# Kernel optimization log

Hardware: AMD Instinct MI355X
Metric: run time of the kernel (lower is better)

## Reference

```python
import jax, jax.numpy as jnp
import numpy as np

IN_FEATURES = 512
OUT_FEATURES = 1024
BATCH = 1024
LAMBD = 0.2
TOL = 1e-4
MAX_ITERS = 100


def setup_inputs() -> dict:
    key = jax.random.key(0)
    kx, kw = jax.random.split(key)
    x = jax.random.normal(kx, (BATCH, IN_FEATURES), dtype=jnp.float32)
    # weight ~ randn(out, in), normalized over dim=0 (per-column) as in torch
    w = jax.random.normal(kw, (OUT_FEATURES, IN_FEATURES), dtype=jnp.float32)
    w = w / jnp.linalg.norm(w, axis=0)
    # M_inv = inverse(A^T A + I)^T with A = weight.T of shape (N, M)
    A = w.T  # (N, M)
    Mmat = A.T @ A + jnp.eye(OUT_FEATURES, dtype=jnp.float32)  # (M, M)
    M_inv = jnp.linalg.inv(Mmat).T
    return {"x": x, "weight": w, "M_inv": M_inv}


def _softshrink(x, lambd):
    return jnp.sign(x) * jnp.maximum(jnp.abs(x) - lambd, 0.0)


def _admm(A_dot_b, M_inv, lambd):
    # Fixed-length scan with per-sample freeze masks, equivalent to the
    # torch loop that removes converged rows from the active batch.
    B, M = A_dot_b.shape
    z = jnp.zeros((B, M), A_dot_b.dtype)
    solved0 = jnp.zeros((B,), dtype=bool)
    # carry: (v, u, v_prev, v_solution, solved)
    def step(carry, _):
        v, u, v_prev, v_sol, solved = carry
        b_eff = A_dot_b + v - u               # (B, M)
        xk = b_eff @ M_inv                    # (B, M)
        v_new = _softshrink(xk + u, lambd)
        u_new = u + xk - v_new
        dx_norm = jnp.linalg.norm(v_new - v_prev, axis=1)
        x_norm = jnp.linalg.norm(v_new, axis=1)
        conv = (dx_norm / x_norm) < TOL       # nan (0/0) compares False, as torch
        newly = conv & (~solved)
        v_sol = jnp.where(newly[:, None], v_new, v_sol)
        solved = solved | newly
        active = ~solved
        # frozen (solved) rows stop updating, mirroring removal from the batch
        v2 = jnp.where(active[:, None], v_new, v)
        u2 = jnp.where(active[:, None], u_new, u)
        return (v2, u2, v2, v_sol, solved), None

    carry0 = (z, z, z, z, solved0)
    (v, u, v_prev, v_sol, solved), _ = jax.lax.scan(step, carry0, None, length=MAX_ITERS)
    # torch returns v_solution (zeros for never-converged samples)
    return v_sol


def reference(x, weight, M_inv):
    input_shape = x.shape
    b = jax.lax.stop_gradient(x.reshape(x.shape[0], -1))  # x.detach().flatten(1)
    A_dot_b = b @ weight.T  # b @ A with A = weight.T -> (B, M)
    encoded = _admm(A_dot_b, M_inv, LAMBD)  # (B, M)
    decoded = encoded @ weight              # (B, N)
    return encoded, decoded.reshape(input_shape)
```

## Files before the change

### kernel.cpp

```cpp
#include <hip/hip_runtime.h>

typedef _Float16 half8 __attribute__((ext_vector_type(8)));
typedef _Float16 half4 __attribute__((ext_vector_type(4)));
typedef float floatx4 __attribute__((ext_vector_type(4)));
typedef float floatx16 __attribute__((ext_vector_type(16)));

static constexpr int BATCH = 1024;
static constexpr int NIN   = 512;
static constexpr int MOUT  = 1024;
static constexpr float LAMBD = 0.2f;
static constexpr float TOLF  = 1e-4f;
static constexpr int MAX_ITERS = 100;
static constexpr int MM = BATCH * MOUT;

__device__ __forceinline__ size_t swz(int idx, int k) {
    return ((((size_t)(idx >> 4) * 32 + (k >> 5)) * 64 +
             ((idx & 15) | (((k >> 3) & 3) << 4))) << 3) + (k & 7);
}

__device__ __forceinline__ size_t swz32(int idx, int k) {
    return ((((size_t)(idx >> 5) * 64 + (k >> 4)) * 64 +
             ((idx & 31) | (((k >> 3) & 1) << 5))) << 3) + (k & 7);
}

__device__ __forceinline__ float shrinkf(float t) {
    float a = fabsf(t) - LAMBD;
    return a > 0.f ? copysignf(a, t) : 0.f;
}

__device__ __forceinline__ void gbar32(int* cnt, int* gen, int seq) {
    __syncthreads();
    if (threadIdx.x == 0) {
        int old = atomicAdd(cnt, 1);
        if (old == seq * 32 - 1) {
            __hip_atomic_store(gen, seq, __ATOMIC_RELAXED,
                               __HIP_MEMORY_SCOPE_AGENT);
        } else {
            while (__hip_atomic_load(gen, __ATOMIC_RELAXED,
                                     __HIP_MEMORY_SCOPE_AGENT) < seq)
                __builtin_amdgcn_s_sleep(1);
        }
    }
    __syncthreads();
    asm volatile("buffer_inv sc0" ::: "memory");
}

__global__ __launch_bounds__(256) void zero_init(float* t, float* enc,
                                                 float* dec, float* ench_f,
                                                 float* encl_f, int* solved) {
    int i = blockIdx.x * 256 + threadIdx.x;
    if (i < MM) { t[i] = 0.f; enc[i] = 0.f; }
    if (i < MM / 2) { dec[i] = 0.f; ench_f[i] = 0.f; encl_f[i] = 0.f; }
    if (i < 4096) solved[i] = 0;
}

__global__ __launch_bounds__(256) void split_minv(const float* __restrict__ Minv,
                                                  _Float16* __restrict__ Th,
                                                  _Float16* __restrict__ Tl) {
    int g = blockIdx.x * 256 + threadIdx.x;
    int n = g & 1023, k0 = (g >> 10) << 3;
    half8 h, l;
    #pragma unroll
    for (int e = 0; e < 8; ++e) {
        float val = Minv[(size_t)(k0 + e) * MOUT + n];
        _Float16 hh = (_Float16)val;
        h[e] = hh;
        l[e] = (_Float16)(val - (float)hh);
    }
    size_t off = swz32(n, k0);
    *(half8*)&Th[off] = h;
    *(half8*)&Tl[off] = l;
}

__global__ __launch_bounds__(256) void split_w(const float* __restrict__ w,
                                               _Float16* __restrict__ wsh,
                                               _Float16* __restrict__ wsl) {
    int g = blockIdx.x * 256 + threadIdx.x;
    int n = g & 511, k0 = (g >> 9) << 3;
    half8 h, l;
    #pragma unroll
    for (int e = 0; e < 8; ++e) {
        float val = w[(size_t)(k0 + e) * NIN + n];
        _Float16 hh = (_Float16)val;
        h[e] = hh;
        l[e] = (_Float16)(val - (float)hh);
    }
    size_t off = swz(n, k0);
    *(half8*)&wsh[off] = h;
    *(half8*)&wsl[off] = l;
}

__global__ __launch_bounds__(256) void gemm_adb(const float* __restrict__ x,
                                                const float* __restrict__ w,
                                                float* __restrict__ adb,
                                                _Float16* __restrict__ bh,
                                                _Float16* __restrict__ bl) {
    __shared__ float As[16][68];
    __shared__ float Bs[16][68];
    const int tid = threadIdx.x;
    const int i0 = (blockIdx.x >> 4) * 64, j0 = (blockIdx.x & 15) * 64;
    const int tx = tid & 15, ty = tid >> 4;
    const int lr = tid >> 2, lk = (tid & 3) << 2;
    float acc[4][4] = {};
    for (int k0 = 0; k0 < NIN; k0 += 16) {
        float4 a4 = *(const float4*)&x[(i0 + lr) * NIN + k0 + lk];
        As[lk + 0][lr] = a4.x; As[lk + 1][lr] = a4.y;
        As[lk + 2][lr] = a4.z; As[lk + 3][lr] = a4.w;
        float4 b4 = *(const float4*)&w[(j0 + lr) * NIN + k0 + lk];
        Bs[lk + 0][lr] = b4.x; Bs[lk + 1][lr] = b4.y;
        Bs[lk + 2][lr] = b4.z; Bs[lk + 3][lr] = b4.w;
        __syncthreads();
        #pragma unroll
        for (int kk = 0; kk < 16; ++kk) {
            float4 a_ = *(const float4*)&As[kk][ty << 2];
            float4 b_ = *(const float4*)&Bs[kk][tx << 2];
            #pragma unroll
            for (int r = 0; r < 4; ++r) {
                float av = r == 0 ? a_.x : r == 1 ? a_.y : r == 2 ? a_.z : a_.w;
                acc[r][0] = fmaf(av, b_.x, acc[r][0]);
                acc[r][1] = fmaf(av, b_.y, acc[r][1]);
                acc[r][2] = fmaf(av, b_.z, acc[r][2]);
                acc[r][3] = fmaf(av, b_.w, acc[r][3]);
            }
        }
        __syncthreads();
    }
    const int k4 = j0 + (tx << 2);
    #pragma unroll
    for (int r = 0; r < 4; ++r) {
        const int row = i0 + (ty << 2) + r;
        *(float4*)&adb[(size_t)row * MOUT + k4] =
            make_float4(acc[r][0], acc[r][1], acc[r][2], acc[r][3]);
        half4 h, l;
        #pragma unroll
        for (int e = 0; e < 4; ++e) {
            _Float16 hh = (_Float16)acc[r][e];
            h[e] = hh;
            l[e] = (_Float16)(acc[r][e] - (float)hh);
        }
        size_t off = swz32(row, k4);
        *(half4*)&bh[off] = h;
        *(half4*)&bl[off] = l;
    }
}

__global__ __launch_bounds__(512, 1)
void admm_loop(const float* __restrict__ adb, float* __restrict__ part,
               _Float16* __restrict__ bh0, _Float16* __restrict__ bl0,
               _Float16* __restrict__ bh1, _Float16* __restrict__ bl1,
               const _Float16* __restrict__ Th, const _Float16* __restrict__ Tl,
               float* __restrict__ enc, _Float16* __restrict__ ench,
               _Float16* __restrict__ encl, int* __restrict__ bar) {
    const int bid = blockIdx.x;
    const int tid = threadIdx.x, lane = tid & 63;
    const int w = tid >> 6;
    const int bt = w >> 1;
    const int kh = w & 1;
    const int mt = bid & 7, nt = bid >> 3;
    const int n0 = nt << 5, m0 = mt << 7;
    const int hn = lane >> 5;
    const int brow = m0 + (bt << 5) + (lane & 31);
    const int btile = (mt << 2) + bt;

    __shared__ _Float16 Bs[128 * 512];
    __shared__ float4 sc4[4][4][64];
    __shared__ unsigned char sfroz[128];

    if (tid < 128) sfroz[tid] = 0;

    #pragma unroll
    for (int q = 0; q < 16; ++q) {
        const int chunk = (w << 4) + q;
        const int kc = chunk >> 1, hl = chunk & 1;
        const _Float16* src = (hl ? Tl : Th) +
            (((size_t)((nt << 6) + kc)) << 9) + ((size_t)lane << 3);
        __builtin_amdgcn_global_load_lds(
            (const __attribute__((address_space(1))) void*)src,
            (__attribute__((address_space(3))) void*)&Bs[(size_t)chunk << 9],
            16, 0, 0);
    }
    __syncthreads();

    int* gcnt = bar + (mt << 5);
    int* ggen = bar + (mt << 5) + 16;

    const int drow_l = (w << 4) + (lane >> 2);
    const int dq = (lane & 3) << 3;
    const float* dbase0 = part + ((((size_t)(m0 + drow_l)) << 6) + (dq << 1));

    float treg[16] = {};
    float adbreg[16];
    #pragma unroll
    for (int r4 = 0; r4 < 4; ++r4) {
        const int nb = n0 + (r4 << 3) + (hn << 2);
        float4 a4 = *(const float4*)&adb[(size_t)brow * MOUT + nb];
        adbreg[(r4 << 2) + 0] = a4.x; adbreg[(r4 << 2) + 1] = a4.y;
        adbreg[(r4 << 2) + 2] = a4.z; adbreg[(r4 << 2) + 3] = a4.w;
    }

    int it = 0;
    for (; it < MAX_ITERS; ++it) {
        const _Float16* rbh = (it & 1) ? bh1 : bh0;
        const _Float16* rbl = (it & 1) ? bl1 : bl0;
        _Float16* wbh = (it & 1) ? bh0 : bh1;
        _Float16* wbl = (it & 1) ? bl0 : bl1;
        const int pw = it & 1;

        float4 dp0, dp1, dp2, dp3;
        if (it) {
            const float* pb = dbase0 + ((size_t)(pw ^ 1) << 16);
            dp0 = *(const float4*)(pb + 0);
            dp1 = *(const float4*)(pb + 4);
            dp2 = *(const float4*)(pb + 8);
            dp3 = *(const float4*)(pb + 12);
        }

        floatx16 accA = {}, accB = {}, accC = {};
        const int kc0 = kh << 5;
        #pragma unroll 4
        for (int kc = kc0; kc < kc0 + 32; ++kc) {
            const size_t boff =
                (((size_t)(btile << 6) + kc) << 9) + ((size_t)lane << 3);
            const half8 bhf = *(const half8*)&rbh[boff];
            const half8 blf = *(const half8*)&rbl[boff];
            const half8 ah = *(const half8*)&Bs[((kc << 1) << 9) + (lane << 3)];
            const half8 al = *(const half8*)&Bs[(((kc << 1) | 1) << 9) + (lane << 3)];
            accA = __builtin_amdgcn_mfma_f32_32x32x16_f16(al, bhf, accA, 0, 0, 0);
            accB = __builtin_amdgcn_mfma_f32_32x32x16_f16(ah, blf, accB, 0, 0, 0);
            accC = __builtin_amdgcn_mfma_f32_32x32x16_f16(ah, bhf, accC, 0, 0, 0);
        }
        if (kh) {
            #pragma unroll
            for (int r4 = 0; r4 < 4; ++r4) {
                float4 v;
                v.x = (accA[(r4 << 2) + 0] + accB[(r4 << 2) + 0]) + accC[(r4 << 2) + 0];
                v.y = (accA[(r4 << 2) + 1] + accB[(r4 << 2) + 1]) + accC[(r4 << 2) + 1];
                v.z = (accA[(r4 << 2) + 2] + accB[(r4 << 2) + 2]) + accC[(r4 << 2) + 2];
                v.w = (accA[(r4 << 2) + 3] + accB[(r4 << 2) + 3]) + accC[(r4 << 2) + 3];
                sc4[bt][r4][lane] = v;
            }
        }

        if (it) {
            float rdx = ((dp0.x + dp0.z) + (dp1.x + dp1.z)) +
                        ((dp2.x + dp2.z) + (dp3.x + dp3.z));
            float rx  = ((dp0.y + dp0.w) + (dp1.y + dp1.w)) +
                        ((dp2.y + dp2.w) + (dp3.y + dp3.w));
            rdx += __shfl_xor(rdx, 1); rdx += __shfl_xor(rdx, 2);
            rx  += __shfl_xor(rx, 1);  rx  += __shfl_xor(rx, 2);
            if (rdx < TOLF * TOLF * rx && (lane & 3) == 0)
                sfroz[drow_l] = 1;
        }
        __syncthreads();

        bool f0 = sfroz[lane] != 0, f1 = sfroz[64 + lane] != 0;
        if ((__ballot(f0) & __ballot(f1)) == ~0ull) break;

        const bool sflag = sfroz[(bt << 5) + (lane & 31)] != 0;
        if (kh == 0 && !sflag) {
            float dx2 = 0.f, x2 = 0.f;
            #pragma unroll
            for (int r4 = 0; r4 < 4; ++r4) {
                float4 p1 = sc4[bt][r4][lane];
                float pa[4] = {p1.x, p1.y, p1.z, p1.w};
                half4 h, l;
                #pragma unroll
                for (int e = 0; e < 4; ++e) {
                    const int r = (r4 << 2) + e;
                    float s0 = (accA[r] + accB[r]) + accC[r];
                    float xk = s0 + pa[e];
                    float t_ = treg[r];
                    float vprev = shrinkf(t_);
                    float uu = t_ - vprev;
                    float tn = xk + uu;
                    float vv = shrinkf(tn);
                    float un = tn - vv;
                    float d = vv - vprev;
                    dx2 += d * d;
                    x2 += vv * vv;
                    treg[r] = tn;
                    float nb_ = (adbreg[r] + vv) - un;
                    _Float16 hh = (_Float16)nb_;
                    h[e] = hh;
                    l[e] = (_Float16)(nb_ - (float)hh);
                }
                size_t off = swz32(brow, n0 + (r4 << 3) + (hn << 2));
                *(half4*)&wbh[off] = h;
                *(half4*)&wbl[off] = l;
            }
            dx2 += __shfl_xor(dx2, 32);
            x2  += __shfl_xor(x2, 32);
            if (hn == 0)
                *(float2*)&part[(((size_t)pw << 16) +
                                 (((size_t)brow) << 6) + ((size_t)nt << 1))] =
                    make_float2(dx2, x2);
        }
        gbar32(gcnt, ggen, it + 1);
    }

    if (it == MAX_ITERS) {
        const float* pb = dbase0 + ((size_t)((MAX_ITERS - 1) & 1) << 16);
        float4 dp0 = *(const float4*)(pb + 0);
        float4 dp1 = *(const float4*)(pb + 4);
        float4 dp2 = *(const float4*)(pb + 8);
        float4 dp3 = *(const float4*)(pb + 12);
        float rdx = ((dp0.x + dp0.z) + (dp1.x + dp1.z)) +
                    ((dp2.x + dp2.z) + (dp3.x + dp3.z));
        float rx  = ((dp0.y + dp0.w) + (dp1.y + dp1.w)) +
                    ((dp2.y + dp2.w) + (dp3.y + dp3.w));
        rdx += __shfl_xor(rdx, 1); rdx += __shfl_xor(rdx, 2);
        rx  += __shfl_xor(rx, 1);  rx  += __shfl_xor(rx, 2);
        if (rdx < TOLF * TOLF * rx && (lane & 3) == 0)
            sfroz[drow_l] = 1;
        __syncthreads();
    }

    if (kh == 0 && sfroz[(bt << 5) + (lane & 31)]) {
        #pragma unroll
        for (int r4 = 0; r4 < 4; ++r4) {
            const int nb = n0 + (r4 << 3) + (hn << 2);
            float va[4]; half4 h, l;
            #pragma unroll
            for (int e = 0; e < 4; ++e) {
                float vv = shrinkf(treg[(r4 << 2) + e]);
                va[e] = vv;
                _Float16 hh = (_Float16)vv;
                h[e] = hh;
                l[e] = (_Float16)(vv - (float)hh);
            }
            *(float4*)&enc[(size_t)brow * MOUT + nb] =
                make_float4(va[0], va[1], va[2], va[3]);
            size_t off = swz(brow, nb);
            *(half4*)&ench[off] = h;
            *(half4*)&encl[off] = l;
        }
    }
}

__global__ __launch_bounds__(256, 2)
void mfma_dec(const _Float16* __restrict__ Ahg, const _Float16* __restrict__ Alg,
              const _Float16* __restrict__ Bhg, const _Float16* __restrict__ Blg,
              float* __restrict__ out) {
    constexpr int NSTR = NIN;
    constexpr int NT = NSTR / 128;
    const int bid = blockIdx.x;
    const int c = bid & 7, t = bid >> 3;
    const int mt = t / NT, nt = t % NT;
    const int tid = threadIdx.x, lane = tid & 63;

    __shared__ _Float16 Ash[64 * 512];

    const int wv = tid >> 6;
    const int wm = (tid >> 7) & 1, wn = (tid >> 6) & 1;
    const int kf0 = c << 2;

    #pragma unroll
    for (int i = 0; i < 16; ++i) {
        const int chunk = (wv << 4) + i;
        const int rt = chunk >> 3, kc = (chunk >> 1) & 3, hl = chunk & 1;
        const _Float16* src = (hl ? Alg : Ahg) +
            ((((size_t)((mt << 3) + rt) * 32 + kf0 + kc) << 9) + ((size_t)lane << 3));
        __builtin_amdgcn_global_load_lds(
            (const __attribute__((address_space(1))) void*)src,
            (__attribute__((address_space(3))) void*)&Ash[(size_t)chunk << 9],
            16, 0, 0);
    }
    __syncthreads();

    const int ct0 = nt * 8 + (wn << 2);
    const _Float16* pBh = Bhg + ((((size_t)ct0 * 32 + kf0) * 64 + lane) << 3);
    const _Float16* pBl = Blg + ((((size_t)ct0 * 32 + kf0) * 64 + lane) << 3);

    floatx4 acc[4][4] = {};
    #pragma unroll
    for (int s = 0; s < 4; ++s) {
        half8 bhf[4], blf[4];
        #pragma unroll
        for (int j = 0; j < 4; ++j) {
            bhf[j] = *(const half8*)(pBh + ((size_t)j << 14) + ((size_t)s << 9));
            blf[j] = *(const half8*)(pBl + ((size_t)j << 14) + ((size_t)s << 9));
        }
        half8 ah[4], al[4];
        #pragma unroll
        for (int i = 0; i < 4; ++i) {
            const int rt = (wm << 2) + i;
            ah[i] = *(const half8*)&Ash[((((rt << 2) + s) << 1) << 9) + (lane << 3)];
            al[i] = *(const half8*)&Ash[(((((rt << 2) + s) << 1) + 1) << 9) + (lane << 3)];
        }
        #pragma unroll
        for (int i = 0; i < 4; ++i)
            #pragma unroll
            for (int j = 0; j < 4; ++j) {
                acc[i][j] = __builtin_amdgcn_mfma_f32_16x16x32_f16(
                    ah[i], blf[j], acc[i][j], 0, 0, 0);
                acc[i][j] = __builtin_amdgcn_mfma_f32_16x16x32_f16(
                    al[i], bhf[j], acc[i][j], 0, 0, 0);
                acc[i][j] = __builtin_amdgcn_mfma_f32_16x16x32_f16(
                    ah[i], bhf[j], acc[i][j], 0, 0, 0);
            }
    }

    const int orow = (lane >> 4) << 2;
    #pragma unroll
    for (int i = 0; i < 4; ++i) {
        const int gr = (mt << 7) + (wm << 6) + (i << 4) + orow;
        #pragma unroll
        for (int j = 0; j < 4; ++j) {
            const int gc = nt * 128 + (wn << 6) + (j << 4) + (lane & 15);
            #pragma unroll
            for (int r = 0; r < 4; ++r)
                atomicAdd(&out[(size_t)(gr + r) * NSTR + gc], acc[i][j][r]);
        }
    }
}

extern "C" void kernel_launch(void* const* d_in, const int* in_sizes, int n_in,
                              void* d_out, int out_size, void* d_ws, size_t ws_size,
                              hipStream_t stream) {
    const float* x    = (const float*)d_in[0];
    const float* w    = (const float*)d_in[1];
    const float* Minv = (const float*)d_in[2];

    float* enc = (float*)d_out;
    float* dec = enc + MM;

    float* ws  = (float*)d_ws;
    float* adb = ws;
    _Float16* bh1 = (_Float16*)(ws + (size_t)MM);
    _Float16* bl1 = bh1 + (size_t)MM;
    float* part = ws + 2 * (size_t)MM;

    _Float16* bh0  = (_Float16*)(ws + 4 * (size_t)MM);
    _Float16* bl0  = bh0 + (size_t)MM;
    _Float16* Th   = bl0 + (size_t)MM;
    _Float16* Tl   = Th + (size_t)MM;
    _Float16* ench = Tl + (size_t)MM;
    _Float16* encl = ench + (size_t)MM;
    _Float16* wsh  = encl + (size_t)MM;
    _Float16* wsl  = wsh + (size_t)(NIN * MOUT);
    int* solved    = (int*)(wsl + (size_t)(NIN * MOUT));
    int* bar       = solved + 1088;

    zero_init<<<(MM + 255) / 256, 256, 0, stream>>>((float*)bh1, enc, dec,
                                                    (float*)ench, (float*)encl,
                                                    solved);
    split_minv<<<512, 256, 0, stream>>>(Minv, Th, Tl);
    split_w<<<256, 256, 0, stream>>>(w, wsh, wsl);
    gemm_adb<<<256, 256, 0, stream>>>(x, w, adb, bh0, bl0);

    void* cargs[] = {(void*)&adb, (void*)&part,
                     (void*)&bh0, (void*)&bl0, (void*)&bh1, (void*)&bl1,
                     (void*)&Th,  (void*)&Tl,
                     (void*)&enc, (void*)&ench, (void*)&encl, (void*)&bar};
    hipLaunchCooperativeKernel(reinterpret_cast<void*>(admm_loop),
                               dim3(256), dim3(512), cargs, 0, stream);

    mfma_dec<<<256, 256, 0, stream>>>(ench, encl, wsh, wsl, dec);
}
```

Measured before the change: 1.038 ms.

## Split K-halves across block pairs with global flag handoff and skip frozen tiles

The work split changes. Before, two waves in each block each took one K-half for one 32-column tile. Now paired blocks take the two K-halves, and each block's two wave-groups cover two column tiles. The K-high block writes its partial sums to a global scratch buffer and raises a per-pair flag, and the K-low block spins on that flag, invalidates its cache and finishes the update. Waves whose 32-row tile is fully frozen also skip their MFMA loop. This adds a global round trip and a spin wait on every iteration, and it leaves half the blocks idle during the elementwise phase.

```diff
diff --git a/kernel.cpp b/kernel.cpp
--- a/kernel.cpp
+++ b/kernel.cpp
@@ -146,6 +146,7 @@
 
 __global__ __launch_bounds__(512, 1)
 void admm_loop(const float* __restrict__ adb, float* __restrict__ part,
+               float* __restrict__ xkx,
                _Float16* __restrict__ bh0, _Float16* __restrict__ bl0,
                _Float16* __restrict__ bh1, _Float16* __restrict__ bl1,
                const _Float16* __restrict__ Th, const _Float16* __restrict__ Tl,
@@ -155,47 +156,60 @@
     const int tid = threadIdx.x, lane = tid & 63;
     const int w = tid >> 6;
     const int bt = w >> 1;
-    const int kh = w & 1;
-    const int mt = bid & 7, nt = bid >> 3;
-    const int n0 = nt << 5, m0 = mt << 7;
+    const int nh = w & 1;
+    const int mt = bid & 7;
+    const int memb = bid >> 3;
+    const int kh = memb & 1;
+    const int ntp = memb >> 1;
+    const int m0 = mt << 7;
+    const int nt2 = (ntp << 1) + nh;
+    const int n0w = nt2 << 5;
     const int hn = lane >> 5;
     const int brow = m0 + (bt << 5) + (lane & 31);
     const int btile = (mt << 2) + bt;
 
     __shared__ _Float16 Bs[128 * 512];
-    __shared__ float4 sc4[4][4][64];
     __shared__ unsigned char sfroz[128];
 
     if (tid < 128) sfroz[tid] = 0;
 
     #pragma unroll
     for (int q = 0; q < 16; ++q) {
-        const int chunk = (w << 4) + q;
-        const int kc = chunk >> 1, hl = chunk & 1;
+        const int c = (w << 4) + q;
+        const int nhc = c >> 6, hl = c & 1, kcp = (c >> 1) & 31;
+        const int snt2 = (ntp << 1) + nhc;
+        const int kc = (kh << 5) + kcp;
         const _Float16* src = (hl ? Tl : Th) +
-            (((size_t)((nt << 6) + kc)) << 9) + ((size_t)lane << 3);
+            (((size_t)(snt2 << 6) + kc) << 9) + ((size_t)lane << 3);
         __builtin_amdgcn_global_load_lds(
             (const __attribute__((address_space(1))) void*)src,
-            (__attribute__((address_space(3))) void*)&Bs[(size_t)chunk << 9],
+            (__attribute__((address_space(3))) void*)&Bs[(size_t)c << 9],
             16, 0, 0);
     }
     __syncthreads();
 
     int* gcnt = bar + (mt << 5);
     int* ggen = bar + (mt << 5) + 16;
+    int* flg  = bar + 256 + (mt << 4) + ntp;
 
     const int drow_l = (w << 4) + (lane >> 2);
     const int dq = (lane & 3) << 3;
     const float* dbase0 = part + ((((size_t)(m0 + drow_l)) << 6) + (dq << 1));
 
+    float* xbase = xkx +
+        (((((size_t)(mt << 4) + ntp) << 2) + bt) * 2 + nh) * 1024 +
+        ((size_t)lane << 2);
+
     float treg[16] = {};
-    float adbreg[16];
-    #pragma unroll
-    for (int r4 = 0; r4 < 4; ++r4) {
-        const int nb = n0 + (r4 << 3) + (hn << 2);
-        float4 a4 = *(const float4*)&adb[(size_t)brow * MOUT + nb];
-        adbreg[(r4 << 2) + 0] = a4.x; adbreg[(r4 << 2) + 1] = a4.y;
-        adbreg[(r4 << 2) + 2] = a4.z; adbreg[(r4 << 2) + 3] = a4.w;
+    float adbreg[16] = {};
+    if (kh == 0) {
+        #pragma unroll
+        for (int r4 = 0; r4 < 4; ++r4) {
+            const int nb = n0w + (r4 << 3) + (hn << 2);
+            float4 a4 = *(const float4*)&adb[(size_t)brow * MOUT + nb];
+            adbreg[(r4 << 2) + 0] = a4.x; adbreg[(r4 << 2) + 1] = a4.y;
+            adbreg[(r4 << 2) + 2] = a4.z; adbreg[(r4 << 2) + 3] = a4.w;
+        }
     }
 
     int it = 0;
@@ -215,29 +229,26 @@
             dp3 = *(const float4*)(pb + 12);
         }
 
+        const bool tfroz =
+            __ballot(sfroz[(bt << 5) + (lane & 31)] != 0) == ~0ull;
+
         floatx16 accA = {}, accB = {}, accC = {};
-        const int kc0 = kh << 5;
-        #pragma unroll 4
-        for (int kc = kc0; kc < kc0 + 32; ++kc) {
-            const size_t boff =
-                (((size_t)(btile << 6) + kc) << 9) + ((size_t)lane << 3);
-            const half8 bhf = *(const half8*)&rbh[boff];
-            const half8 blf = *(const half8*)&rbl[boff];
-            const half8 ah = *(const half8*)&Bs[((kc << 1) << 9) + (lane << 3)];
-            const half8 al = *(const half8*)&Bs[(((kc << 1) | 1) << 9) + (lane << 3)];
-            accA = __builtin_amdgcn_mfma_f32_32x32x16_f16(al, bhf, accA, 0, 0, 0);
-            accB = __builtin_amdgcn_mfma_f32_32x32x16_f16(ah, blf, accB, 0, 0, 0);
-            accC = __builtin_amdgcn_mfma_f32_32x32x16_f16(ah, bhf, accC, 0, 0, 0);
-        }
-        if (kh) {
-            #pragma unroll
-            for (int r4 = 0; r4 < 4; ++r4) {
-                float4 v;
-                v.x = (accA[(r4 << 2) + 0] + accB[(r4 << 2) + 0]) + accC[(r4 << 2) + 0];
-                v.y = (accA[(r4 << 2) + 1] + accB[(r4 << 2) + 1]) + accC[(r4 << 2) + 1];
-                v.z = (accA[(r4 << 2) + 2] + accB[(r4 << 2) + 2]) + accC[(r4 << 2) + 2];
-                v.w = (accA[(r4 << 2) + 3] + accB[(r4 << 2) + 3]) + accC[(r4 << 2) + 3];
-                sc4[bt][r4][lane] = v;
+        if (!tfroz) {
+            const int kc0 = kh << 5;
+            #pragma unroll 4
+            for (int kcp = 0; kcp < 32; ++kcp) {
+                const int kc = kc0 + kcp;
+                const size_t boff =
+                    (((size_t)(btile << 6) + kc) << 9) + ((size_t)lane << 3);
+                const half8 bhf = *(const half8*)&rbh[boff];
+                const half8 blf = *(const half8*)&rbl[boff];
+                const half8 ah = *(const half8*)
+                    &Bs[(((nh << 6) | (kcp << 1)) << 9) + (lane << 3)];
+                const half8 al = *(const half8*)
+                    &Bs[((((nh << 6) | (kcp << 1)) | 1) << 9) + (lane << 3)];
+                accA = __builtin_amdgcn_mfma_f32_32x32x16_f16(al, bhf, accA, 0, 0, 0);
+                accB = __builtin_amdgcn_mfma_f32_32x32x16_f16(ah, blf, accB, 0, 0, 0);
+                accC = __builtin_amdgcn_mfma_f32_32x32x16_f16(ah, bhf, accC, 0, 0, 0);
             }
         }
 
@@ -256,44 +267,70 @@
         bool f0 = sfroz[lane] != 0, f1 = sfroz[64 + lane] != 0;
         if ((__ballot(f0) & __ballot(f1)) == ~0ull) break;
 
-        const bool sflag = sfroz[(bt << 5) + (lane & 31)] != 0;
-        if (kh == 0 && !sflag) {
-            float dx2 = 0.f, x2 = 0.f;
-            #pragma unroll
-            for (int r4 = 0; r4 < 4; ++r4) {
-                float4 p1 = sc4[bt][r4][lane];
-                float pa[4] = {p1.x, p1.y, p1.z, p1.w};
-                half4 h, l;
+        if (kh) {
+            if (!tfroz) {
                 #pragma unroll
-                for (int e = 0; e < 4; ++e) {
-                    const int r = (r4 << 2) + e;
-                    float s0 = (accA[r] + accB[r]) + accC[r];
-                    float xk = s0 + pa[e];
-                    float t_ = treg[r];
-                    float vprev = shrinkf(t_);
-                    float uu = t_ - vprev;
-                    float tn = xk + uu;
-                    float vv = shrinkf(tn);
-                    float un = tn - vv;
-                    float d = vv - vprev;
-                    dx2 += d * d;
-                    x2 += vv * vv;
-                    treg[r] = tn;
-                    float nb_ = (adbreg[r] + vv) - un;
-                    _Float16 hh = (_Float16)nb_;
-                    h[e] = hh;
-                    l[e] = (_Float16)(nb_ - (float)hh);
+                for (int r4 = 0; r4 < 4; ++r4) {
+                    float4 v;
+                    v.x = (accA[(r4 << 2) + 0] + accB[(r4 << 2) + 0]) + accC[(r4 << 2) + 0];
+                    v.y = (accA[(r4 << 2) + 1] + accB[(r4 << 2) + 1]) + accC[(r4 << 2) + 1];
+                    v.z = (accA[(r4 << 2) + 2] + accB[(r4 << 2) + 2]) + accC[(r4 << 2) + 2];
+                    v.w = (accA[(r4 << 2) + 3] + accB[(r4 << 2) + 3]) + accC[(r4 << 2) + 3];
+                    *(float4*)&xbase[r4 << 8] = v;
                 }
-                size_t off = swz32(brow, n0 + (r4 << 3) + (hn << 2));
-                *(half4*)&wbh[off] = h;
-                *(half4*)&wbl[off] = l;
-            }
-            dx2 += __shfl_xor(dx2, 32);
-            x2  += __shfl_xor(x2, 32);
-            if (hn == 0)
-                *(float2*)&part[(((size_t)pw << 16) +
-                                 (((size_t)brow) << 6) + ((size_t)nt << 1))] =
-                    make_float2(dx2, x2);
+            }
+            __syncthreads();
+            if (tid == 0)
+                __hip_atomic_store(flg, it + 1, __ATOMIC_RELAXED,
+                                   __HIP_MEMORY_SCOPE_AGENT);
+        } else {
+            if (tid == 0) {
+                while (__hip_atomic_load(flg, __ATOMIC_RELAXED,
+                                         __HIP_MEMORY_SCOPE_AGENT) < it + 1)
+                    __builtin_amdgcn_s_sleep(1);
+            }
+            __syncthreads();
+            asm volatile("buffer_inv sc0" ::: "memory");
+            const bool sflag = sfroz[(bt << 5) + (lane & 31)] != 0;
+            if (!sflag) {
+                float dx2 = 0.f, x2 = 0.f;
+                #pragma unroll
+                for (int r4 = 0; r4 < 4; ++r4) {
+                    float4 p1 = *(const float4*)&xbase[r4 << 8];
+                    float pa[4] = {p1.x, p1.y, p1.z, p1.w};
+                    half4 h, l;
+                    #pragma unroll
+                    for (int e = 0; e < 4; ++e) {
+                        const int r = (r4 << 2) + e;
+                        float s0 = (accA[r] + accB[r]) + accC[r];
+                        float xk = s0 + pa[e];
+                        float t_ = treg[r];
+                        float vprev = shrinkf(t_);
+                        float uu = t_ - vprev;
+                        float tn = xk + uu;
+                        float vv = shrinkf(tn);
+                        float un = tn - vv;
+                        float d = vv - vprev;
+                        dx2 += d * d;
+                        x2 += vv * vv;
+                        treg[r] = tn;
+                        float nb_ = (adbreg[r] + vv) - un;
+                        _Float16 hh = (_Float16)nb_;
+                        h[e] = hh;
+                        l[e] = (_Float16)(nb_ - (float)hh);
+                    }
+                    size_t off = swz32(brow, n0w + (r4 << 3) + (hn << 2));
+                    *(half4*)&wbh[off] = h;
+                    *(half4*)&wbl[off] = l;
+                }
+                dx2 += __shfl_xor(dx2, 32);
+                x2  += __shfl_xor(x2, 32);
+                if (hn == 0)
+                    *(float2*)&part[(((size_t)pw << 16) +
+                                     (((size_t)brow) << 6) +
+                                     ((size_t)nt2 << 1))] =
+                        make_float2(dx2, x2);
+            }
         }
         gbar32(gcnt, ggen, it + 1);
     }
@@ -318,7 +355,7 @@
     if (kh == 0 && sfroz[(bt << 5) + (lane & 31)]) {
         #pragma unroll
         for (int r4 = 0; r4 < 4; ++r4) {
-            const int nb = n0 + (r4 << 3) + (hn << 2);
+            const int nb = n0w + (r4 << 3) + (hn << 2);
             float va[4]; half4 h, l;
             #pragma unroll
             for (int e = 0; e < 4; ++e) {
@@ -429,6 +466,7 @@
     _Float16* bh1 = (_Float16*)(ws + (size_t)MM);
     _Float16* bl1 = bh1 + (size_t)MM;
     float* part = ws + 2 * (size_t)MM;
+    float* xkx  = part + 262144;
 
     _Float16* bh0  = (_Float16*)(ws + 4 * (size_t)MM);
     _Float16* bl0  = bh0 + (size_t)MM;
@@ -448,7 +486,7 @@
     split_w<<<256, 256, 0, stream>>>(w, wsh, wsl);
     gemm_adb<<<256, 256, 0, stream>>>(x, w, adb, bh0, bl0);
 
-    void* cargs[] = {(void*)&adb, (void*)&part,
+    void* cargs[] = {(void*)&adb, (void*)&part, (void*)&xkx,
                      (void*)&bh0, (void*)&bl0, (void*)&bh1, (void*)&bl1,
                      (void*)&Th,  (void*)&Tl,
                      (void*)&enc, (void*)&ench, (void*)&encl, (void*)&bar};
```

Result: slower. 1.365 ms (+31.5%).
